# Optimization experiments

Measured on AMD Instinct MI355X. Metric: run time of the kernel, lower is better.

## Reference

```python
import jax, jax.numpy as jnp
import numpy as np

IN_FEATURES = 2048
OUT_FEATURES = 2048
NNZ = 262144
N_NODES = 65536


def setup_inputs() -> dict:
    key = jax.random.key(0)
    k_x, k_v, k_b, k_r, k_c = jax.random.split(key, 5)
    x = jax.random.normal(k_x, (N_NODES, IN_FEATURES), dtype=jnp.float32)
    values = jax.random.normal(k_v, (NNZ,), dtype=jnp.float32)
    bias_param = jax.random.normal(k_b, (OUT_FEATURES,), dtype=jnp.float32)
    rows = jax.random.randint(k_r, (NNZ,), 0, OUT_FEATURES, dtype=jnp.int32)
    cols = jax.random.randint(k_c, (NNZ,), 0, IN_FEATURES, dtype=jnp.int32)
    return {"x": x, "values": values, "bias_param": bias_param,
            "rows": rows, "cols": cols}


def reference(x, values, bias_param, rows, cols):
    # Scatter COO values into the dense [out, in] weight (sum semantics for
    # any duplicate coordinates, matching sparse spmm accumulation), then
    # y = spmm(W_sparse, x.T).T == x @ W.T + bias.
    W = jnp.zeros((OUT_FEATURES, IN_FEATURES), dtype=values.dtype)
    W = W.at[rows, cols].add(values)
    return jnp.einsum('ni,oi->no', x, W) + bias_param
```

## Files before the change

### kernel.cpp

```cpp
#include <hip/hip_runtime.h>


#define M_DIM 65536
#define K_DIM 2048
#define N_DIM 2048
#define NNZ_CNT 262144

typedef short bf16x8 __attribute__((ext_vector_type(8)));
typedef float f32x4 __attribute__((ext_vector_type(4)));
typedef unsigned int u32x4 __attribute__((ext_vector_type(4)));

__device__ __forceinline__ unsigned short f2bf(float f) {
  union { float f; unsigned u; } v; v.f = f;
  unsigned r = v.u + 0x7fffu + ((v.u >> 16) & 1u);
  return (unsigned short)(r >> 16);
}

__device__ __forceinline__ void glds16(const void* g, const void* l) {
  __builtin_amdgcn_global_load_lds(
      (const __attribute__((address_space(1))) void*)g,
      (__attribute__((address_space(3))) void*)l, 16, 0, 0);
}

__global__ void scatter_kernel(float* __restrict__ W, const float* __restrict__ vals,
                               const int* __restrict__ rows, const int* __restrict__ cols) {
  int i = blockIdx.x * 256 + threadIdx.x;
  atomicAdd(&W[(size_t)rows[i] * K_DIM + cols[i]], vals[i]);
}

__global__ void cvt_kernel(const float* __restrict__ in, unsigned short* __restrict__ out) {
  size_t i = ((size_t)blockIdx.x * 256 + threadIdx.x) * 8;
  f32x4 a = *(const f32x4*)(in + i);
  f32x4 b = *(const f32x4*)(in + i + 4);
  u32x4 p;
  p.x = f2bf(a.x) | ((unsigned)f2bf(a.y) << 16);
  p.y = f2bf(a.z) | ((unsigned)f2bf(a.w) << 16);
  p.z = f2bf(b.x) | ((unsigned)f2bf(b.y) << 16);
  p.w = f2bf(b.z) | ((unsigned)f2bf(b.w) << 16);
  *(u32x4*)(out + i) = p;
}

template <bool PRECONV>
__global__ __launch_bounds__(256) void gemm_kernel(
    const float* __restrict__ xf, const unsigned short* __restrict__ xb,
    const unsigned short* __restrict__ wb, const float* __restrict__ bias,
    float* __restrict__ out) {
  __shared__ __align__(16) unsigned short lsA[128 * 32];
  __shared__ __align__(16) unsigned short lsB[128 * 32];
  const int tid = threadIdx.x;
  const int lane = tid & 63;
  const int wave = tid >> 6;
  const int m0 = blockIdx.y * 128;
  const int n0 = blockIdx.x * 128;
  const int r = lane & 15;
  const int q = lane >> 4;
  const int wm = (wave & 1) * 64;
  const int wn = (wave >> 1) * 64;

  f32x4 acc[4][4] = {};

  const int srow = wave * 16 + (lane >> 2);
  const int scol = (lane & 3) * 8;

  for (int kt = 0; kt < K_DIM / 32; ++kt) {
    const int kb = kt * 32;
    if (PRECONV) {
#pragma unroll
      for (int i = 0; i < 2; ++i) {
        const unsigned short* g =
            xb + (size_t)(m0 + i * 64 + srow) * K_DIM + kb + scol;
        glds16(g, lsA + i * 2048 + wave * 512);
      }
    } else {
      const int row = tid >> 1;
      const int ce = (tid & 1) * 16;
      const float* g = xf + (size_t)(m0 + row) * K_DIM + kb + ce;
      f32x4 f0 = ((const f32x4*)g)[0];
      f32x4 f1 = ((const f32x4*)g)[1];
      f32x4 f2 = ((const f32x4*)g)[2];
      f32x4 f3 = ((const f32x4*)g)[3];
      u32x4 p0, p1;
      p0.x = f2bf(f0.x) | ((unsigned)f2bf(f0.y) << 16);
      p0.y = f2bf(f0.z) | ((unsigned)f2bf(f0.w) << 16);
      p0.z = f2bf(f1.x) | ((unsigned)f2bf(f1.y) << 16);
      p0.w = f2bf(f1.z) | ((unsigned)f2bf(f1.w) << 16);
      p1.x = f2bf(f2.x) | ((unsigned)f2bf(f2.y) << 16);
      p1.y = f2bf(f2.z) | ((unsigned)f2bf(f2.w) << 16);
      p1.z = f2bf(f3.x) | ((unsigned)f2bf(f3.y) << 16);
      p1.w = f2bf(f3.z) | ((unsigned)f2bf(f3.w) << 16);
      *(u32x4*)(lsA + row * 32 + ce) = p0;
      *(u32x4*)(lsA + row * 32 + ce + 8) = p1;
    }
#pragma unroll
    for (int i = 0; i < 2; ++i) {
      const unsigned short* g =
          wb + (size_t)(n0 + i * 64 + srow) * K_DIM + kb + scol;
      glds16(g, lsB + i * 2048 + wave * 512);
    }
    __syncthreads();

    bf16x8 af[4], bfr[4];
#pragma unroll
    for (int mi = 0; mi < 4; ++mi)
      af[mi] = *(const bf16x8*)(lsA + (wm + mi * 16 + r) * 32 + q * 8);
#pragma unroll
    for (int ni = 0; ni < 4; ++ni)
      bfr[ni] = *(const bf16x8*)(lsB + (wn + ni * 16 + r) * 32 + q * 8);
#pragma unroll
    for (int mi = 0; mi < 4; ++mi)
#pragma unroll
      for (int ni = 0; ni < 4; ++ni)
        acc[mi][ni] = __builtin_amdgcn_mfma_f32_16x16x32_bf16(
            af[mi], bfr[ni], acc[mi][ni], 0, 0, 0);
    __syncthreads();
  }

#pragma unroll
  for (int ni = 0; ni < 4; ++ni) {
    const int n = n0 + wn + ni * 16 + r;
    const float bv = bias[n];
#pragma unroll
    for (int mi = 0; mi < 4; ++mi) {
      const int mbase = m0 + wm + mi * 16 + q * 4;
#pragma unroll
      for (int reg = 0; reg < 4; ++reg)
        out[(size_t)(mbase + reg) * N_DIM + n] = acc[mi][ni][reg] + bv;
    }
  }
}

extern "C" void kernel_launch(void* const* d_in, const int* in_sizes, int n_in,
                              void* d_out, int out_size, void* d_ws, size_t ws_size,
                              hipStream_t stream) {
  const float* x = (const float*)d_in[0];
  const float* values = (const float*)d_in[1];
  const float* bias = (const float*)d_in[2];
  const int* rows = (const int*)d_in[3];
  const int* cols = (const int*)d_in[4];
  float* out = (float*)d_out;

  unsigned char* ws = (unsigned char*)d_ws;
  float* Wf = (float*)ws;
  unsigned short* Wb = (unsigned short*)(ws + (16u << 20));
  unsigned short* Xb = (unsigned short*)(ws + (24u << 20));

  hipMemsetAsync(Wf, 0, (size_t)N_DIM * K_DIM * sizeof(float), stream);
  scatter_kernel<<<NNZ_CNT / 256, 256, 0, stream>>>(Wf, values, rows, cols);
  cvt_kernel<<<(N_DIM * K_DIM) / 2048, 256, 0, stream>>>(Wf, Wb);

  const size_t need = (24u << 20) + (size_t)M_DIM * K_DIM * 2;
  dim3 grid(N_DIM / 128, M_DIM / 128);
  if (ws_size >= need) {
    cvt_kernel<<<((size_t)M_DIM * K_DIM) / 2048, 256, 0, stream>>>(x, Xb);
    gemm_kernel<true><<<grid, 256, 0, stream>>>(nullptr, Xb, Wb, bias, out);
  } else {
    gemm_kernel<false><<<grid, 256, 0, stream>>>(x, nullptr, Wb, bias, out);
  }
}
```

Before: 1.516 ms.

## Replace GEMM with 256x256 double-buffered, swizzled, ping-pong scheduled bf16 kernel

Replaces the preconverted-path GEMM with a 512-thread kernel computing 256x256 output tiles with a K-step of 64. Global-to-LDS loads are double buffered and interleaved with MFMA phases using explicit barriers, vmcnt/lgkmcnt waits and s_setprio. LDS uses an XOR swizzle to avoid bank conflicts, and block IDs are remapped so neighbouring blocks share tiles in L2. The goal is to hide load latency and raise data reuse per LDS byte, at the cost of large LDS use (about 129 KB per block), fragile hand-placed waits, and dummy loads on the last iteration.

```diff
diff --git a/kernel.cpp b/kernel.cpp
--- a/kernel.cpp
+++ b/kernel.cpp
@@ -40,11 +40,139 @@
   *(u32x4*)(out + i) = p;
 }
 
-template <bool PRECONV>
-__global__ __launch_bounds__(256) void gemm_kernel(
-    const float* __restrict__ xf, const unsigned short* __restrict__ xb,
-    const unsigned short* __restrict__ wb, const float* __restrict__ bias,
-    float* __restrict__ out) {
+
+#define BARF() do { asm volatile("" ::: "memory"); __builtin_amdgcn_s_barrier(); \
+                    asm volatile("" ::: "memory"); } while (0)
+#define WAIT_LGKM0() asm volatile("s_waitcnt lgkmcnt(0)" ::: "memory")
+#define WAIT_VM4()   asm volatile("s_waitcnt vmcnt(4)" ::: "memory")
+#define PRIO1() __builtin_amdgcn_s_setprio(1)
+#define PRIO0() __builtin_amdgcn_s_setprio(0)
+
+__global__ __launch_bounds__(512, 2) void gemm256_kernel(
+    const unsigned short* __restrict__ xb, const unsigned short* __restrict__ wb,
+    const float* __restrict__ bias, float* __restrict__ out) {
+  __shared__ __align__(16) unsigned char lds[131072 + 1024];
+  const int tid = threadIdx.x;
+  const int lane = tid & 63;
+  const int wave = tid >> 6;
+  const int wm = wave >> 2;
+  const int wn = wave & 3;
+  const int r = lane & 15;
+  const int q = lane >> 4;
+
+  const int bid = blockIdx.x;
+  const int v = (bid & 7) * 256 + (bid >> 3);
+  const int m0 = (v >> 3) * 256;
+  const int n0 = (v & 7) * 256;
+
+  const int srow = wave * 8 + (lane >> 3);
+  const int scb = ((lane & 7) ^ (lane >> 3)) << 3;
+  const unsigned short* Ab = xb + (size_t)(m0 + srow) * K_DIM + scb;
+  const unsigned short* Bb = wb + (size_t)(n0 + srow) * K_DIM + scb;
+  unsigned char* lw = lds + wave * 1024;
+
+  const int swx = (r & 7) << 4;
+  const int cb0 = (q << 4) ^ swx;
+  const int cb1 = (64 | (q << 4)) ^ swx;
+
+  f32x4 acc[8][4] = {};
+  bf16x8 av[4][2];
+  bf16x8 bA[2][2];
+  bf16x8 bB[2][2];
+
+#define STAGE(kt, h, bufbyte) do {                                              \
+    const unsigned short* g_ = (((h) & 2) ? Bb : Ab)                            \
+        + (size_t)(((h) & 1) * 128) * K_DIM + (kt) * 64;                        \
+    unsigned char* l_ = lw + (bufbyte) + ((h) & 2) * 16384 + ((h) & 1) * 16384; \
+    glds16(g_, l_);                                                             \
+    glds16(g_ + (size_t)64 * K_DIM, l_ + 8192);                                 \
+  } while (0)
+#define STAGE_DUMMY() do { glds16(Ab, lds + 131072); glds16(Ab, lds + 131072); } while (0)
+
+#define LDA4(base, mh) do { _Pragma("unroll") for (int i_ = 0; i_ < 4; ++i_) {  \
+    const int rb_ = (wm * 128 + (mh) * 64 + i_ * 16 + r) * 128;                 \
+    av[i_][0] = *(const bf16x8*)(lds + (base) + rb_ + cb0);                     \
+    av[i_][1] = *(const bf16x8*)(lds + (base) + rb_ + cb1); } } while (0)
+
+#define LDB2(dst, base, nh) do { _Pragma("unroll") for (int i_ = 0; i_ < 2; ++i_) { \
+    const int rb_ = (wn * 64 + (nh) * 32 + i_ * 16 + r) * 128;                  \
+    dst[i_][0] = *(const bf16x8*)(lds + (base) + 32768 + rb_ + cb0);            \
+    dst[i_][1] = *(const bf16x8*)(lds + (base) + 32768 + rb_ + cb1); } } while (0)
+
+#define MQ(mh, bb, nh) do { _Pragma("unroll") for (int i_ = 0; i_ < 4; ++i_)    \
+    _Pragma("unroll") for (int j_ = 0; j_ < 2; ++j_) {                          \
+      acc[(mh)*4+i_][(nh)*2+j_] = __builtin_amdgcn_mfma_f32_16x16x32_bf16(      \
+          av[i_][0], bb[j_][0], acc[(mh)*4+i_][(nh)*2+j_], 0, 0, 0);            \
+      acc[(mh)*4+i_][(nh)*2+j_] = __builtin_amdgcn_mfma_f32_16x16x32_bf16(      \
+          av[i_][1], bb[j_][1], acc[(mh)*4+i_][(nh)*2+j_], 0, 0, 0); } } while (0)
+
+  STAGE(0, 0, 0); STAGE(0, 1, 0); STAGE(0, 2, 0); STAGE(0, 3, 0);
+  STAGE(1, 0, 65536); STAGE(1, 1, 65536);
+  WAIT_VM4();
+  BARF();
+
+  for (int it = 0; it < 16; ++it) {
+    const int t1 = 2 * it + 1;
+    const bool lastit = (it == 15);
+    LDA4(0, 0); LDB2(bA, 0, 0);
+    STAGE(t1, 2, 65536);
+    BARF(); WAIT_LGKM0();
+    PRIO1(); MQ(0, bA, 0); PRIO0();
+    BARF();
+    LDB2(bB, 0, 1);
+    STAGE(t1, 3, 65536);
+    BARF(); WAIT_LGKM0();
+    PRIO1(); MQ(0, bB, 1); PRIO0();
+    BARF();
+    LDA4(0, 1);
+    BARF(); WAIT_LGKM0();
+    PRIO1(); MQ(1, bB, 1); PRIO0();
+    BARF();
+    if (!lastit) { STAGE(t1 + 1, 0, 0); STAGE(t1 + 1, 1, 0); }
+    else { STAGE_DUMMY(); STAGE_DUMMY(); }
+    BARF();
+    PRIO1(); MQ(1, bA, 0); PRIO0();
+    WAIT_VM4();
+    BARF();
+    LDA4(65536, 0); LDB2(bA, 65536, 0);
+    if (!lastit) STAGE(t1 + 1, 2, 0); else STAGE_DUMMY();
+    BARF(); WAIT_LGKM0();
+    PRIO1(); MQ(0, bA, 0); PRIO0();
+    BARF();
+    LDB2(bB, 65536, 1);
+    if (!lastit) STAGE(t1 + 1, 3, 0); else STAGE_DUMMY();
+    BARF(); WAIT_LGKM0();
+    PRIO1(); MQ(0, bB, 1); PRIO0();
+    BARF();
+    LDA4(65536, 1);
+    BARF(); WAIT_LGKM0();
+    PRIO1(); MQ(1, bB, 1); PRIO0();
+    BARF();
+    if (!lastit) { STAGE(t1 + 2, 0, 65536); STAGE(t1 + 2, 1, 65536); }
+    else { STAGE_DUMMY(); STAGE_DUMMY(); }
+    BARF();
+    PRIO1(); MQ(1, bA, 0); PRIO0();
+    WAIT_VM4();
+    BARF();
+  }
+
+#pragma unroll
+  for (int ni = 0; ni < 4; ++ni) {
+    const int n = n0 + wn * 64 + ni * 16 + r;
+    const float bv = bias[n];
+#pragma unroll
+    for (int mi = 0; mi < 8; ++mi) {
+      const size_t mb = (size_t)(m0 + wm * 128 + mi * 16 + q * 4) * N_DIM + n;
+#pragma unroll
+      for (int rg = 0; rg < 4; ++rg)
+        out[mb + (size_t)rg * N_DIM] = acc[mi][ni][rg] + bv;
+    }
+  }
+}
+
+__global__ __launch_bounds__(256) void gemm_fallback(
+    const float* __restrict__ xf, const unsigned short* __restrict__ wb,
+    const float* __restrict__ bias, float* __restrict__ out) {
   __shared__ __align__(16) unsigned short lsA[128 * 32];
   __shared__ __align__(16) unsigned short lsB[128 * 32];
   const int tid = threadIdx.x;
@@ -56,22 +184,13 @@
   const int q = lane >> 4;
   const int wm = (wave & 1) * 64;
   const int wn = (wave >> 1) * 64;
-
   f32x4 acc[4][4] = {};
-
   const int srow = wave * 16 + (lane >> 2);
   const int scol = (lane & 3) * 8;
 
   for (int kt = 0; kt < K_DIM / 32; ++kt) {
     const int kb = kt * 32;
-    if (PRECONV) {
-#pragma unroll
-      for (int i = 0; i < 2; ++i) {
-        const unsigned short* g =
-            xb + (size_t)(m0 + i * 64 + srow) * K_DIM + kb + scol;
-        glds16(g, lsA + i * 2048 + wave * 512);
-      }
-    } else {
+    {
       const int row = tid >> 1;
       const int ce = (tid & 1) * 16;
       const float* g = xf + (size_t)(m0 + row) * K_DIM + kb + ce;
@@ -98,7 +217,6 @@
       glds16(g, lsB + i * 2048 + wave * 512);
     }
     __syncthreads();
-
     bf16x8 af[4], bfr[4];
 #pragma unroll
     for (int mi = 0; mi < 4; ++mi)
@@ -114,7 +232,6 @@
             af[mi], bfr[ni], acc[mi][ni], 0, 0, 0);
     __syncthreads();
   }
-
 #pragma unroll
   for (int ni = 0; ni < 4; ++ni) {
     const int n = n0 + wn + ni * 16 + r;
@@ -149,11 +266,11 @@
   cvt_kernel<<<(N_DIM * K_DIM) / 2048, 256, 0, stream>>>(Wf, Wb);
 
   const size_t need = (24u << 20) + (size_t)M_DIM * K_DIM * 2;
-  dim3 grid(N_DIM / 128, M_DIM / 128);
   if (ws_size >= need) {
     cvt_kernel<<<((size_t)M_DIM * K_DIM) / 2048, 256, 0, stream>>>(x, Xb);
-    gemm_kernel<true><<<grid, 256, 0, stream>>>(nullptr, Xb, Wb, bias, out);
+    gemm256_kernel<<<(M_DIM / 256) * (N_DIM / 256), 512, 0, stream>>>(Xb, Wb, bias, out);
   } else {
-    gemm_kernel<false><<<grid, 256, 0, stream>>>(x, nullptr, Wb, bias, out);
-  }
-}
+    dim3 grid(N_DIM / 128, M_DIM / 128);
+    gemm_fallback<<<grid, 256, 0, stream>>>(x, Wb, bias, out);
+  }
+}
```

Result: faster. 1.322 ms (-12.8%).
